# Kernel tuning notes

Hardware: AMD Instinct MI355X
Metric: run time of the kernel (lower is better)

Reference implementation:

```python
import jax, jax.numpy as jnp
import numpy as np

DETER, STOCH, ACT, HID, OBS = 1024, 32, 6, 1024, 1024
B, T = 256, 64

def _lin(x, w, b):
    return x @ w.T + b

def setup_inputs() -> dict:
    key = jax.random.key(0)
    ks = iter(jax.random.split(key, 40))
    def p(shape, scale=0.02):
        return (jax.random.normal(next(ks), shape, dtype=jnp.float32) * scale)
    inp = {
        "obs": jax.random.normal(next(ks), (B, T, OBS), dtype=jnp.float32),
        "actions": jax.random.normal(next(ks), (B, T, ACT), dtype=jnp.float32),
        "eps_prior": jax.random.normal(next(ks), (B, T, STOCH), dtype=jnp.float32),
        "eps_post": jax.random.normal(next(ks), (B, T, STOCH), dtype=jnp.float32),
        # input_mlp
        "in_w1": p((HID, STOCH + ACT)), "in_b1": p((HID,)),
        "in_w2": p((HID, HID)), "in_b2": p((HID,)),
        # GRUCell (torch layout: r,z,n chunks)
        "gru_wih": p((3 * DETER, HID)), "gru_whh": p((3 * DETER, DETER)),
        "gru_bih": p((3 * DETER,)), "gru_bhh": p((3 * DETER,)),
        # prior
        "pr_w1": p((HID, DETER)), "pr_b1": p((HID,)),
        "pr_w2": p((HID, HID)), "pr_b2": p((HID,)),
        "pr_mw": p((STOCH, HID)), "pr_mb": p((STOCH,)),
        "pr_sw": p((STOCH, HID)), "pr_sb": p((STOCH,)),
        # posterior
        "po_w1": p((HID, DETER + OBS)), "po_b1": p((HID,)),
        "po_w2": p((HID, HID)), "po_b2": p((HID,)),
        "po_mw": p((STOCH, HID)), "po_mb": p((STOCH,)),
        "po_sw": p((STOCH, HID)), "po_sb": p((STOCH,)),
    }
    return inp

def _rollout(obs, actions, eps_prior, eps_post,
             in_w1, in_b1, in_w2, in_b2,
             gru_wih, gru_whh, gru_bih, gru_bhh,
             pr_w1, pr_b1, pr_w2, pr_b2, pr_mw, pr_mb, pr_sw, pr_sb,
             po_w1, po_b1, po_w2, po_b2, po_mw, po_mb, po_sw, po_sb):
    Bn = obs.shape[0]
    h0 = jnp.zeros((Bn, DETER), obs.dtype)
    z0 = jnp.zeros((Bn, STOCH), obs.dtype)
    a0 = jnp.zeros((Bn, ACT), obs.dtype)

    def step(carry, xs):
        h, z, prev_a = carry
        obs_t, act_t, ep, eq = xs
        x = jnp.concatenate([z, prev_a], axis=-1)
        x = jax.nn.relu(_lin(x, in_w1, in_b1))
        x = jax.nn.relu(_lin(x, in_w2, in_b2))
        # GRUCell
        gi = _lin(x, gru_wih, gru_bih)
        gh = _lin(h, gru_whh, gru_bhh)
        ir, iz, inn = jnp.split(gi, 3, axis=-1)
        hr, hz, hn = jnp.split(gh, 3, axis=-1)
        r = jax.nn.sigmoid(ir + hr)
        u = jax.nn.sigmoid(iz + hz)
        n = jnp.tanh(inn + r * hn)
        h_new = (1.0 - u) * n + u * h
        # prior
        px = jax.nn.relu(_lin(h_new, pr_w1, pr_b1))
        px = jax.nn.relu(_lin(px, pr_w2, pr_b2))
        p_mean = _lin(px, pr_mw, pr_mb)
        p_std = jnp.exp(jnp.clip(_lin(px, pr_sw, pr_sb), -5.0, 2.0))
        # posterior
        qx = jnp.concatenate([h_new, obs_t], axis=-1)
        qx = jax.nn.relu(_lin(qx, po_w1, po_b1))
        qx = jax.nn.relu(_lin(qx, po_w2, po_b2))
        q_mean = _lin(qx, po_mw, po_mb)
        q_std = jnp.exp(jnp.clip(_lin(qx, po_sw, po_sb), -5.0, 2.0))
        z_new = q_mean + q_std * eq
        feat = jnp.concatenate([h_new, z_new], axis=-1)
        return (h_new, z_new, act_t), (feat, p_mean, p_std, q_mean, q_std)

    xs = (jnp.swapaxes(obs, 0, 1), jnp.swapaxes(actions, 0, 1),
          jnp.swapaxes(eps_prior, 0, 1), jnp.swapaxes(eps_post, 0, 1))
    _, (feat, pm, ps, qm, qs) = jax.lax.scan(step, (h0, z0, a0), xs)
    to_bt = lambda a: jnp.swapaxes(a, 0, 1)  # [T,B,...] -> [B,T,...]
    return to_bt(feat), to_bt(pm), to_bt(ps), to_bt(qm), to_bt(qs)

def reference(obs, actions, eps_prior, eps_post,
              in_w1, in_b1, in_w2, in_b2,
              gru_wih, gru_whh, gru_bih, gru_bhh,
              pr_w1, pr_b1, pr_w2, pr_b2, pr_mw, pr_mb, pr_sw, pr_sb,
              po_w1, po_b1, po_w2, po_b2, po_mw, po_mb, po_sw, po_sb):
    return _rollout(obs, actions, eps_prior, eps_post,
                    in_w1, in_b1, in_w2, in_b2,
                    gru_wih, gru_whh, gru_bih, gru_bhh,
                    pr_w1, pr_b1, pr_w2, pr_b2, pr_mw, pr_mb, pr_sw, pr_sb,
                    po_w1, po_b1, po_w2, po_b2, po_mw, po_mb, po_sw, po_sb)
```

## Files before the change

kernel.cpp:

```cpp
#include <hip/hip_runtime.h>
#include <hip/hip_bf16.h>

#define B_   256
#define T_   64
#define OBS_ 1024
#define ACT_ 6
#define STO_ 32
#define HID_ 1024
#define DET_ 1024

using bf16 = __bf16;
typedef __attribute__((ext_vector_type(8))) __bf16 bf16x8;
typedef __attribute__((ext_vector_type(4))) float f32x4;

__device__ __forceinline__ f32x4 MF(bf16x8 a, bf16x8 b, f32x4 c) {
  return __builtin_amdgcn_mfma_f32_16x16x32_bf16(a, b, c, 0, 0, 0);
}

struct CvtArgs {
  const float *in_w2, *gru_wih, *gru_whh, *pr_w1, *pr_w2, *po_w1, *po_w2;
  const float *pr_mw, *pr_sw, *po_mw, *po_sw;
  bf16 *w_in2b, *w_wihb, *w_whhb, *w_pr1b, *w_pr2b, *w_po1hb, *w_po1ob, *w_po2b, *w_headb;
};

__global__ void k_cvtall(CvtArgs a) {
  const int row = blockIdx.x;
  const float* src; bf16* dst; int srcld = 1024, off = 0;
  if      (row < 1024)  { src = a.in_w2   + (size_t)row * 1024;          dst = a.w_in2b  + (size_t)row * 1024; }
  else if (row < 4096)  { int r = row - 1024;  src = a.gru_wih + (size_t)r * 1024; dst = a.w_wihb + (size_t)r * 1024; }
  else if (row < 7168)  { int r = row - 4096;  src = a.gru_whh + (size_t)r * 1024; dst = a.w_whhb + (size_t)r * 1024; }
  else if (row < 8192)  { int r = row - 7168;  src = a.pr_w1   + (size_t)r * 1024; dst = a.w_pr1b + (size_t)r * 1024; }
  else if (row < 9216)  { int r = row - 8192;  src = a.pr_w2   + (size_t)r * 1024; dst = a.w_pr2b + (size_t)r * 1024; }
  else if (row < 10240) { int r = row - 9216;  src = a.po_w1   + (size_t)r * 2048; dst = a.w_po1hb + (size_t)r * 1024; }
  else if (row < 11264) { int r = row - 10240; src = a.po_w1   + (size_t)r * 2048 + 1024; dst = a.w_po1ob + (size_t)r * 1024; }
  else if (row < 12288) { int r = row - 11264; src = a.po_w2   + (size_t)r * 1024; dst = a.w_po2b + (size_t)r * 1024; }
  else {
    int r = row - 12288;
    const float* hs[4] = { a.pr_mw, a.pr_sw, a.po_mw, a.po_sw };
    src = hs[r >> 5] + (size_t)(r & 31) * 1024;
    dst = a.w_headb + (size_t)r * 1024;
  }
  const int c = threadIdx.x * 4;
  float4 f = *(const float4*)(src + c);
  dst[c] = (bf16)f.x; dst[c + 1] = (bf16)f.y; dst[c + 2] = (bf16)f.z; dst[c + 3] = (bf16)f.w;
}

__global__ void k_init(const float* __restrict__ in_b1, bf16* __restrict__ x1b,
                       bf16* __restrict__ hb, float* __restrict__ hf) {
  const int i = blockIdx.x * 256 + threadIdx.x;
  x1b[i] = (bf16)fmaxf(in_b1[i & 1023], 0.f);
  hb[i] = (bf16)0.f;
  hf[i] = 0.f;
}

__global__ __launch_bounds__(256) void k_qbatch(
    const float* __restrict__ obs, const bf16* __restrict__ w,
    const float* __restrict__ bias, float* __restrict__ out) {
  const int tid = threadIdx.x, lane = tid & 63, wv = tid >> 6;
  const int l15 = lane & 15, kg = lane >> 4, kq = kg * 8, rq = kg * 4;
  const int m0 = (blockIdx.x & 255) * 64 + wv * 16;
  const int n0 = (blockIdx.x >> 8) * 64;
  f32x4 c0{0.f,0.f,0.f,0.f}, c1 = c0, c2 = c0, c3 = c0;
  const float* __restrict__ ap = obs + (size_t)(m0 + l15) * 1024 + kq;
  const bf16* __restrict__ wp = w + (size_t)(n0 + l15) * 1024 + kq;
  #pragma unroll 2
  for (int k = 0; k < 1024; k += 32) {
    float4 f0 = *(const float4*)(ap + k);
    float4 f1 = *(const float4*)(ap + k + 4);
    bf16x8 af;
    af[0] = (bf16)f0.x; af[1] = (bf16)f0.y; af[2] = (bf16)f0.z; af[3] = (bf16)f0.w;
    af[4] = (bf16)f1.x; af[5] = (bf16)f1.y; af[6] = (bf16)f1.z; af[7] = (bf16)f1.w;
    c0 = MF(af, *(const bf16x8*)(wp + k            ), c0);
    c1 = MF(af, *(const bf16x8*)(wp + 16 * 1024 + k), c1);
    c2 = MF(af, *(const bf16x8*)(wp + 32 * 1024 + k), c2);
    c3 = MF(af, *(const bf16x8*)(wp + 48 * 1024 + k), c3);
  }
  f32x4 cc[4] = {c0, c1, c2, c3};
  #pragma unroll
  for (int t2 = 0; t2 < 4; ++t2) {
    const int n = n0 + t2 * 16 + l15;
    const float bv = bias[n];
    #pragma unroll
    for (int r = 0; r < 4; ++r)
      out[(size_t)(m0 + rq + r) * 1024 + n] = cc[t2][r] + bv;
  }
}

struct GB {
  const bf16* A;
  const bf16* W;
  const float* bias;
  const float* acc;
  bf16* outB;
  float* outF;
  int N, lda, relu, accStride;
};

__global__ __launch_bounds__(256, 4) void k_mgs(GB g0, GB g1, int s1) {
  GB g; int tile;
  if ((int)blockIdx.x < s1) { g = g0; tile = blockIdx.x; }
  else                      { g = g1; tile = blockIdx.x - s1; }
  __shared__ float sh[3 * 1056];
  const int tid = threadIdx.x, lane = tid & 63, kw = tid >> 6;
  const int l15 = lane & 15, kg = lane >> 4, kq = kg * 8, rq = kg * 4;
  const int m0 = (tile & 15) * 16;
  const int n0 = (tile >> 4) * 64;

  f32x4 c0{0.f,0.f,0.f,0.f}, c1 = c0, c2 = c0, c3 = c0;
  const bf16* __restrict__ ap = g.A + (size_t)(m0 + l15) * g.lda + kw * 256 + kq;
  const bf16* __restrict__ wp = g.W + (size_t)(n0 + l15) * 1024 + kw * 256 + kq;
  #pragma unroll
  for (int k = 0; k < 256; k += 32) {
    bf16x8 af = *(const bf16x8*)(ap + k);
    c0 = MF(af, *(const bf16x8*)(wp + k            ), c0);
    c1 = MF(af, *(const bf16x8*)(wp + 16 * 1024 + k), c1);
    c2 = MF(af, *(const bf16x8*)(wp + 32 * 1024 + k), c2);
    c3 = MF(af, *(const bf16x8*)(wp + 48 * 1024 + k), c3);
  }
  f32x4 cc[4] = {c0, c1, c2, c3};
  if (kw) {
    float* s = sh + (kw - 1) * 1056;
    #pragma unroll
    for (int t2 = 0; t2 < 4; ++t2)
      #pragma unroll
      for (int r = 0; r < 4; ++r)
        s[(rq + r) * 66 + t2 * 16 + l15] = cc[t2][r];
  }
  __syncthreads();
  if (kw == 0) {
    #pragma unroll
    for (int t2 = 0; t2 < 4; ++t2) {
      const int n = n0 + t2 * 16 + l15;
      const float bv = g.bias ? g.bias[n] : 0.f;
      #pragma unroll
      for (int r = 0; r < 4; ++r) {
        const int row = m0 + rq + r;
        float v = cc[t2][r] + bv;
        #pragma unroll
        for (int s = 0; s < 3; ++s)
          v += sh[s * 1056 + (rq + r) * 66 + t2 * 16 + l15];
        if (g.acc) v += g.acc[(size_t)row * g.accStride + n];
        if (g.relu) v = fmaxf(v, 0.f);
        if (g.outB) g.outB[(size_t)row * g.N + n] = (bf16)v;
        if (g.outF) g.outF[(size_t)row * g.N + n] = v;
      }
    }
  }
}

__global__ __launch_bounds__(256, 4) void k_gates2(
    const bf16* __restrict__ x2b, const bf16* __restrict__ wihb,
    const float* __restrict__ bih, const float* __restrict__ gh,
    float* __restrict__ hf, bf16* __restrict__ hb, float* __restrict__ feat, int t) {
  __shared__ float sh[3 * 816];
  const int mt = blockIdx.x & 15, cs = blockIdx.x >> 4;
  const int tid = threadIdx.x, lane = tid & 63, kw = tid >> 6;
  const int l15 = lane & 15, kg = lane >> 4, kq = kg * 8, rq = kg * 4;

  f32x4 ar{0.f,0.f,0.f,0.f}, az = ar, an = ar;
  const bf16* __restrict__ ap = x2b + (size_t)(mt * 16 + l15) * 1024 + kw * 256 + kq;
  const bf16* __restrict__ wr = wihb + (size_t)(cs * 16 + l15) * 1024 + kw * 256 + kq;
  const size_t GOFF = (size_t)1024 * 1024;
  #pragma unroll
  for (int k = 0; k < 256; k += 32) {
    bf16x8 af = *(const bf16x8*)(ap + k);
    ar = MF(af, *(const bf16x8*)(wr + k           ), ar);
    az = MF(af, *(const bf16x8*)(wr + GOFF + k    ), az);
    an = MF(af, *(const bf16x8*)(wr + 2 * GOFF + k), an);
  }
  if (kw) {
    float* s = sh + (kw - 1) * 816;
    #pragma unroll
    for (int r = 0; r < 4; ++r) {
      s[(rq + r) * 17 + l15]             = ar[r];
      s[272 + (rq + r) * 17 + l15]       = az[r];
      s[544 + (rq + r) * 17 + l15]       = an[r];
    }
  }
  __syncthreads();
  if (kw == 0) {
    const int c = cs * 16 + l15;
    const float bir = bih[c], biz = bih[1024 + c], bin_ = bih[2048 + c];
    #pragma unroll
    for (int r = 0; r < 4; ++r) {
      float vr = ar[r], vz = az[r], vn = an[r];
      #pragma unroll
      for (int s = 0; s < 3; ++s) {
        vr += sh[s * 816 + (rq + r) * 17 + l15];
        vz += sh[s * 816 + 272 + (rq + r) * 17 + l15];
        vn += sh[s * 816 + 544 + (rq + r) * 17 + l15];
      }
      const int m = mt * 16 + rq + r;
      const float* ghp = gh + (size_t)m * 3072 + c;
      float rr = vr + bir + ghp[0];
      float zz = vz + biz + ghp[1024];
      const float hn = ghp[2048];
      rr = 1.f / (1.f + __expf(-rr));
      zz = 1.f / (1.f + __expf(-zz));
      const float nn = tanhf(vn + bin_ + rr * hn);
      const float h2 = (1.f - zz) * nn + zz * hf[(size_t)m * 1024 + c];
      hf[(size_t)m * 1024 + c] = h2;
      hb[(size_t)m * 1024 + c] = (bf16)h2;
      feat[((size_t)m * T_ + t) * 1056 + c] = h2;
    }
  }
}

__global__ __launch_bounds__(1024, 1) void k_headfin2(
    const bf16* __restrict__ p2b, const bf16* __restrict__ q2b,
    const bf16* __restrict__ whead,
    const float* __restrict__ pr_mb, const float* __restrict__ pr_sb,
    const float* __restrict__ po_mb, const float* __restrict__ po_sb,
    const float* __restrict__ eps, const float* __restrict__ act,
    const float* __restrict__ in_w1, const float* __restrict__ in_b1,
    float* __restrict__ pm, float* __restrict__ ps,
    float* __restrict__ qm, float* __restrict__ qs,
    float* __restrict__ feat, bf16* __restrict__ x1b, int t) {
  __shared__ float sh[8 * 1056];
  __shared__ float zm[16][32], zs[16][32], zl[16][32], al[16][8];
  const int g = blockIdx.x, m0 = g * 16;
  const int tid = threadIdx.x, lane = tid & 63, w = tid >> 6;
  const int l15 = lane & 15, kg = lane >> 4, kq = kg * 8, rq = kg * 4;

  if (w < 8) {
    const int kw = w & 3, half = w >> 2;
    const bf16* __restrict__ A = half ? q2b : p2b;
    f32x4 c0{0.f,0.f,0.f,0.f}, c1 = c0, c2 = c0, c3 = c0;
    const bf16* __restrict__ ap = A + (size_t)(m0 + l15) * 1024 + kw * 256 + kq;
    const bf16* __restrict__ wp = whead + (size_t)(half * 64 + l15) * 1024 + kw * 256 + kq;
    #pragma unroll
    for (int k = 0; k < 256; k += 32) {
      bf16x8 af = *(const bf16x8*)(ap + k);
      c0 = MF(af, *(const bf16x8*)(wp + k            ), c0);
      c1 = MF(af, *(const bf16x8*)(wp + 16 * 1024 + k), c1);
      c2 = MF(af, *(const bf16x8*)(wp + 32 * 1024 + k), c2);
      c3 = MF(af, *(const bf16x8*)(wp + 48 * 1024 + k), c3);
    }
    f32x4 cc[4] = {c0, c1, c2, c3};
    float* s = sh + w * 1056;
    #pragma unroll
    for (int t2 = 0; t2 < 4; ++t2)
      #pragma unroll
      for (int r = 0; r < 4; ++r)
        s[(rq + r) * 66 + t2 * 16 + l15] = cc[t2][r];
  }
  if (tid >= 928 && tid < 1024) {
    const int idx = tid - 928, r = idx / ACT_, k = idx - r * ACT_;
    al[r][k] = act[((size_t)(m0 + r) * T_ + t) * ACT_ + k];
  }
  __syncthreads();

  #pragma unroll
  for (int rep = 0; rep < 2; ++rep) {
    const int idx = rep * 1024 + tid;
    const int r = idx >> 7, c = idx & 127;
    const int base = (c < 64) ? 0 : 4, cl = c & 63;
    float v = sh[base * 1056 + r * 66 + cl] + sh[(base + 1) * 1056 + r * 66 + cl]
            + sh[(base + 2) * 1056 + r * 66 + cl] + sh[(base + 3) * 1056 + r * 66 + cl];
    const size_t ob = ((size_t)(m0 + r) * T_ + t) * STO_ + (c & 31);
    const int sel = c >> 5;
    if (sel == 0) {
      pm[ob] = v + pr_mb[c];
    } else if (sel == 1) {
      ps[ob] = __expf(fminf(fmaxf(v + pr_sb[c - 32], -5.f), 2.f));
    } else if (sel == 2) {
      const float x = v + po_mb[c - 64];
      qm[ob] = x; zm[r][c - 64] = x;
    } else {
      const float x = __expf(fminf(fmaxf(v + po_sb[c - 96], -5.f), 2.f));
      qs[ob] = x; zs[r][c - 96] = x;
    }
  }
  __syncthreads();
  if (tid < 512) {
    const int r = tid >> 5, j = tid & 31;
    const float z = zm[r][j] + zs[r][j] * eps[((size_t)(m0 + r) * T_ + t) * STO_ + j];
    zl[r][j] = z;
    feat[((size_t)(m0 + r) * T_ + t) * 1056 + 1024 + j] = z;
  }
  __syncthreads();

  const int n = tid;
  float wv_[38];
  #pragma unroll
  for (int j = 0; j < 38; ++j) wv_[j] = in_w1[(size_t)n * 38 + j];
  const float bn = in_b1[n];
  #pragma unroll 2
  for (int r = 0; r < 16; ++r) {
    float a = bn;
    #pragma unroll
    for (int k = 0; k < STO_; ++k) a = fmaf(zl[r][k], wv_[k], a);
    #pragma unroll
    for (int k = 0; k < ACT_; ++k) a = fmaf(al[r][k], wv_[32 + k], a);
    x1b[(size_t)(m0 + r) * 1024 + n] = (bf16)fmaxf(a, 0.f);
  }
}

extern "C" void kernel_launch(void* const* d_in, const int* in_sizes, int n_in,
                              void* d_out, int out_size, void* d_ws, size_t ws_size,
                              hipStream_t stream) {
  (void)in_sizes; (void)n_in; (void)out_size; (void)ws_size;
  const float* obs      = (const float*)d_in[0];
  const float* actions  = (const float*)d_in[1];
  const float* eps_post = (const float*)d_in[3];
  const float* in_w1 = (const float*)d_in[4];
  const float* in_b1 = (const float*)d_in[5];
  const float* in_w2 = (const float*)d_in[6];
  const float* in_b2 = (const float*)d_in[7];
  const float* gru_wih = (const float*)d_in[8];
  const float* gru_whh = (const float*)d_in[9];
  const float* gru_bih = (const float*)d_in[10];
  const float* gru_bhh = (const float*)d_in[11];
  const float* pr_w1 = (const float*)d_in[12];
  const float* pr_b1 = (const float*)d_in[13];
  const float* pr_w2 = (const float*)d_in[14];
  const float* pr_b2 = (const float*)d_in[15];
  const float* pr_mw = (const float*)d_in[16];
  const float* pr_mb = (const float*)d_in[17];
  const float* pr_sw = (const float*)d_in[18];
  const float* pr_sb = (const float*)d_in[19];
  const float* po_w1 = (const float*)d_in[20];
  const float* po_b1 = (const float*)d_in[21];
  const float* po_w2 = (const float*)d_in[22];
  const float* po_b2 = (const float*)d_in[23];
  const float* po_mw = (const float*)d_in[24];
  const float* po_mb = (const float*)d_in[25];
  const float* po_sw = (const float*)d_in[26];
  const float* po_sb = (const float*)d_in[27];

  float* feat = (float*)d_out;
  float* pm = feat + (size_t)B_ * T_ * 1056;
  float* ps = pm + (size_t)B_ * T_ * STO_;
  float* qm = ps + (size_t)B_ * T_ * STO_;
  float* qs = qm + (size_t)B_ * T_ * STO_;

  char* wp_ = (char*)d_ws;
  auto carve = [&](size_t bytes) -> void* {
    void* r = (void*)wp_;
    wp_ += (bytes + 255) & ~(size_t)255;
    return r;
  };
  bf16* w_in2b  = (bf16*)carve((size_t)HID_ * HID_ * 2);
  bf16* w_wihb  = (bf16*)carve((size_t)3 * DET_ * HID_ * 2);
  bf16* w_whhb  = (bf16*)carve((size_t)3 * DET_ * DET_ * 2);
  bf16* w_pr1b  = (bf16*)carve((size_t)HID_ * DET_ * 2);
  bf16* w_pr2b  = (bf16*)carve((size_t)HID_ * HID_ * 2);
  bf16* w_po1hb = (bf16*)carve((size_t)HID_ * DET_ * 2);
  bf16* w_po1ob = (bf16*)carve((size_t)HID_ * OBS_ * 2);
  bf16* w_po2b  = (bf16*)carve((size_t)HID_ * HID_ * 2);
  bf16* w_headb = (bf16*)carve((size_t)128 * HID_ * 2);
  bf16* x1b  = (bf16*)carve((size_t)B_ * HID_ * 2);
  bf16* x2b  = (bf16*)carve((size_t)B_ * HID_ * 2);
  bf16* hb   = (bf16*)carve((size_t)B_ * DET_ * 2);
  bf16* p1b  = (bf16*)carve((size_t)B_ * HID_ * 2);
  bf16* q1b  = (bf16*)carve((size_t)B_ * HID_ * 2);
  bf16* p2b  = (bf16*)carve((size_t)B_ * HID_ * 2);
  bf16* q2b  = (bf16*)carve((size_t)B_ * HID_ * 2);
  float* hf       = (float*)carve((size_t)B_ * DET_ * 4);
  float* gh       = (float*)carve((size_t)B_ * 3 * DET_ * 4);
  float* q1acc    = (float*)carve((size_t)B_ * T_ * HID_ * 4);

  CvtArgs ca = { in_w2, gru_wih, gru_whh, pr_w1, pr_w2, po_w1, po_w2,
                 pr_mw, pr_sw, po_mw, po_sw,
                 w_in2b, w_wihb, w_whhb, w_pr1b, w_pr2b, w_po1hb, w_po1ob, w_po2b, w_headb };
  k_cvtall<<<dim3(12416), dim3(256), 0, stream>>>(ca);
  k_init<<<dim3(1024), dim3(256), 0, stream>>>(in_b1, x1b, hb, hf);
  k_qbatch<<<dim3(4096), dim3(256), 0, stream>>>(obs, w_po1ob, po_b1, q1acc);

  for (int t = 0; t < T_; ++t) {
    GB g_x2 = { x1b, w_in2b, in_b2,   nullptr, x2b, nullptr, 1024, 1024, 1, 0 };
    GB g_gh = { hb,  w_whhb, gru_bhh, nullptr, nullptr, gh, 3072, 1024, 0, 0 };
    k_mgs<<<dim3(1024), dim3(256), 0, stream>>>(g_x2, g_gh, 256);

    k_gates2<<<dim3(1024), dim3(256), 0, stream>>>(x2b, w_wihb, gru_bih, gh, hf, hb, feat, t);

    GB g_pr1 = { hb, w_pr1b,  pr_b1,   nullptr,           p1b, nullptr, 1024, 1024, 1, 0 };
    GB g_q1  = { hb, w_po1hb, nullptr, q1acc + t * 1024,  q1b, nullptr, 1024, 1024, 1, T_ * 1024 };
    k_mgs<<<dim3(512), dim3(256), 0, stream>>>(g_pr1, g_q1, 256);

    GB g_pr2 = { p1b, w_pr2b, pr_b2, nullptr, p2b, nullptr, 1024, 1024, 1, 0 };
    GB g_po2 = { q1b, w_po2b, po_b2, nullptr, q2b, nullptr, 1024, 1024, 1, 0 };
    k_mgs<<<dim3(512), dim3(256), 0, stream>>>(g_pr2, g_po2, 256);

    k_headfin2<<<dim3(16), dim3(1024), 0, stream>>>(
        p2b, q2b, w_headb, pr_mb, pr_sb, po_mb, po_sb,
        eps_post, actions, in_w1, in_b1, pm, ps, qm, qs, feat, x1b, t);
  }
}
```

Baseline: 6.055 ms.

## Fuse per-step kernels into one dataflow kernel with atomic counters

Replaces the four kernel launches per timestep with a single 240-block kernel. Block groups specialise by stage (input MLP, GRU, prior/posterior layers, heads) and hand off row tiles through global atomic counters instead of kernel boundaries. The GRU recurrent matmul runs before waiting on the input MLP, so the two overlap, and the h state is double-buffered so blocks can read the previous state while the new one is written. Correctness depends on all 240 blocks being co-resident, since waiting blocks spin, and each stage now runs on fewer, larger tiles with full-K loops and no split-K.

Result: slower. 15.04 ms (+148.3%).

```diff
diff --git a/kernel.cpp b/kernel.cpp
--- a/kernel.cpp
+++ b/kernel.cpp
@@ -7,7 +7,6 @@
 #define ACT_ 6
 #define STO_ 32
 #define HID_ 1024
-#define DET_ 1024
 
 using bf16 = __bf16;
 typedef __attribute__((ext_vector_type(8))) __bf16 bf16x8;
@@ -15,6 +14,272 @@
 
 __device__ __forceinline__ f32x4 MF(bf16x8 a, bf16x8 b, f32x4 c) {
   return __builtin_amdgcn_mfma_f32_16x16x32_bf16(a, b, c, 0, 0, 0);
+}
+
+__device__ __forceinline__ void waitctr(unsigned* c, unsigned tgt) {
+  if ((threadIdx.x & 63) == 0) {
+    while (__hip_atomic_load(c, __ATOMIC_RELAXED, __HIP_MEMORY_SCOPE_AGENT) < tgt)
+      __builtin_amdgcn_s_sleep(1);
+    __hip_atomic_load(c, __ATOMIC_ACQUIRE, __HIP_MEMORY_SCOPE_AGENT);
+  }
+  __builtin_amdgcn_wave_barrier();
+  asm volatile("" ::: "memory");
+}
+__device__ __forceinline__ void signalctr(unsigned* c) {
+  __syncthreads();
+  if (threadIdx.x == 0)
+    __hip_atomic_fetch_add(c, 1u, __ATOMIC_RELEASE, __HIP_MEMORY_SCOPE_AGENT);
+}
+
+__device__ __forceinline__ void gemm128(
+    const bf16* __restrict__ A, int m0,
+    const bf16* __restrict__ W,
+    const float* __restrict__ bias,
+    const float* __restrict__ accb, size_t accLd,
+    bf16* __restrict__ outb, int ldo) {
+  const int tid = threadIdx.x, lane = tid & 63, wv = tid >> 6;
+  const int l15 = lane & 15, kg = lane >> 4, kq = kg << 3, rq = kg << 2;
+  const int mrow = m0 + (wv & 3) * 16;
+  const int nb = (wv >> 2) * 64;
+  f32x4 a0{0.f,0.f,0.f,0.f}, a1 = a0, a2 = a0, a3 = a0;
+  const bf16* __restrict__ ap = A + (size_t)(mrow + l15) * 1024 + kq;
+  const bf16* __restrict__ wp = W + (size_t)(nb + l15) * 1024 + kq;
+  #pragma unroll 4
+  for (int k = 0; k < 1024; k += 32) {
+    bf16x8 af = *(const bf16x8*)(ap + k);
+    a0 = MF(af, *(const bf16x8*)(wp + k            ), a0);
+    a1 = MF(af, *(const bf16x8*)(wp + 16*1024 + k  ), a1);
+    a2 = MF(af, *(const bf16x8*)(wp + 32*1024 + k  ), a2);
+    a3 = MF(af, *(const bf16x8*)(wp + 48*1024 + k  ), a3);
+  }
+  f32x4 aa[4] = {a0, a1, a2, a3};
+  #pragma unroll
+  for (int nf = 0; nf < 4; ++nf) {
+    const int col = nb + nf * 16 + l15;
+    const float bv = bias ? bias[col] : 0.f;
+    #pragma unroll
+    for (int r = 0; r < 4; ++r) {
+      const int row = mrow + rq + r;
+      float v = aa[nf][r] + bv;
+      if (accb) v += accb[(size_t)row * accLd + col];
+      v = fmaxf(v, 0.f);
+      outb[(size_t)row * ldo + col] = (bf16)v;
+    }
+  }
+}
+
+struct SPar {
+  const bf16 *w_in2, *w_wih, *w_whh, *w_pr1, *w_po1h, *w_pr2, *w_po2, *w_head;
+  const float *b_in2, *b_ih, *b_hh, *b_pr1, *b_pr2, *b_po2;
+  const float *pr_mb, *pr_sb, *po_mb, *po_sb;
+  const float *eps, *act, *in_w1, *in_b1;
+  bf16 *x1b, *x2b, *p1b, *q1b, *p2b, *q2b, *hbA, *hbB;
+  float *hfA, *hfB;
+  const float *q1acc;
+  float *feat, *pm, *ps, *qm, *qs;
+  unsigned *ctr;
+};
+
+__global__ __launch_bounds__(512) void k_step(SPar P, int t) {
+  __shared__ float shmem[10048];
+  const int bid = blockIdx.x, tid = threadIdx.x;
+  const int lane = tid & 63, wv = tid >> 6;
+  const int l15 = lane & 15, kg = lane >> 4, kq = kg << 3, rq = kg << 2;
+  unsigned* cc = P.ctr + t * 32;
+  bf16* hbCur  = (t & 1) ? P.hbB : P.hbA;
+  const bf16* hbPrev = (t & 1) ? P.hbA : P.hbB;
+  float* hfCur = (t & 1) ? P.hfB : P.hfA;
+  const float* hfPrev = (t & 1) ? P.hfA : P.hfB;
+
+  if (bid < 32) {
+    const int mt = bid & 3, nt = bid >> 2;
+    gemm128(P.x1b, mt * 64, P.w_in2 + (size_t)nt * 128 * 1024,
+            P.b_in2 + nt * 128, nullptr, 0, P.x2b + nt * 128, 1024);
+    signalctr(&cc[0 * 4 + mt]);
+
+  } else if (bid < 96) {
+    const int idx = bid - 32, mt = idx & 3, cs = idx >> 2;
+    const int msub = wv & 3, nsh = wv >> 2;
+    const int mrow = mt * 64 + msub * 16;
+    const int cb = cs * 64 + nsh * 32;
+    f32x4 gh[3][2], gi[3][2];
+    #pragma unroll
+    for (int g = 0; g < 3; ++g)
+      #pragma unroll
+      for (int nf = 0; nf < 2; ++nf) { gh[g][nf] = f32x4{0.f,0.f,0.f,0.f}; gi[g][nf] = gh[g][nf]; }
+
+    {
+      const bf16* __restrict__ ap = hbPrev + (size_t)(mrow + l15) * 1024 + kq;
+      const bf16* wr[3][2];
+      #pragma unroll
+      for (int g = 0; g < 3; ++g)
+        #pragma unroll
+        for (int nf = 0; nf < 2; ++nf)
+          wr[g][nf] = P.w_whh + (size_t)(g * 1024 + cb + nf * 16 + l15) * 1024 + kq;
+      #pragma unroll 2
+      for (int k = 0; k < 1024; k += 32) {
+        bf16x8 af = *(const bf16x8*)(ap + k);
+        #pragma unroll
+        for (int g = 0; g < 3; ++g)
+          #pragma unroll
+          for (int nf = 0; nf < 2; ++nf)
+            gh[g][nf] = MF(af, *(const bf16x8*)(wr[g][nf] + k), gh[g][nf]);
+      }
+    }
+    waitctr(&cc[0 * 4 + mt], 8);
+    {
+      const bf16* __restrict__ ap = P.x2b + (size_t)(mrow + l15) * 1024 + kq;
+      const bf16* wr[3][2];
+      #pragma unroll
+      for (int g = 0; g < 3; ++g)
+        #pragma unroll
+        for (int nf = 0; nf < 2; ++nf)
+          wr[g][nf] = P.w_wih + (size_t)(g * 1024 + cb + nf * 16 + l15) * 1024 + kq;
+      #pragma unroll 2
+      for (int k = 0; k < 1024; k += 32) {
+        bf16x8 af = *(const bf16x8*)(ap + k);
+        #pragma unroll
+        for (int g = 0; g < 3; ++g)
+          #pragma unroll
+          for (int nf = 0; nf < 2; ++nf)
+            gi[g][nf] = MF(af, *(const bf16x8*)(wr[g][nf] + k), gi[g][nf]);
+      }
+    }
+    #pragma unroll
+    for (int nf = 0; nf < 2; ++nf) {
+      const int col = cb + nf * 16 + l15;
+      const float bir = P.b_ih[col], biz = P.b_ih[1024 + col], bin_ = P.b_ih[2048 + col];
+      const float bhr = P.b_hh[col], bhz = P.b_hh[1024 + col], bhn = P.b_hh[2048 + col];
+      #pragma unroll
+      for (int r = 0; r < 4; ++r) {
+        const int row = mrow + rq + r;
+        float rr = gi[0][nf][r] + bir + gh[0][nf][r] + bhr;
+        float zz = gi[1][nf][r] + biz + gh[1][nf][r] + bhz;
+        const float hn = gh[2][nf][r] + bhn;
+        rr = 1.f / (1.f + __expf(-rr));
+        zz = 1.f / (1.f + __expf(-zz));
+        const float nn = tanhf(gi[2][nf][r] + bin_ + rr * hn);
+        const float h2 = (1.f - zz) * nn + zz * hfPrev[(size_t)row * 1024 + col];
+        hbCur[(size_t)row * 1024 + col] = (bf16)h2;
+        hfCur[(size_t)row * 1024 + col] = h2;
+        P.feat[((size_t)row * T_ + t) * 1056 + col] = h2;
+      }
+    }
+    signalctr(&cc[1 * 4 + mt]);
+
+  } else if (bid < 128) {
+    const int idx = bid - 96, mt = idx & 3, nt = idx >> 2;
+    waitctr(&cc[1 * 4 + mt], 16);
+    gemm128(hbCur, mt * 64, P.w_po1h + (size_t)nt * 128 * 1024, nullptr,
+            P.q1acc + (size_t)t * 1024 + nt * 128, (size_t)T_ * 1024,
+            P.q1b + nt * 128, 1024);
+    signalctr(&cc[2 * 4 + mt]);
+
+  } else if (bid < 160) {
+    const int idx = bid - 128, mt = idx & 3, nt = idx >> 2;
+    waitctr(&cc[1 * 4 + mt], 16);
+    gemm128(hbCur, mt * 64, P.w_pr1 + (size_t)nt * 128 * 1024,
+            P.b_pr1 + nt * 128, nullptr, 0, P.p1b + nt * 128, 1024);
+    signalctr(&cc[3 * 4 + mt]);
+
+  } else if (bid < 192) {
+    const int idx = bid - 160, mt = idx & 3, nt = idx >> 2;
+    waitctr(&cc[2 * 4 + mt], 8);
+    gemm128(P.q1b, mt * 64, P.w_po2 + (size_t)nt * 128 * 1024,
+            P.b_po2 + nt * 128, nullptr, 0, P.q2b + nt * 128, 1024);
+    signalctr(&cc[4 * 4 + mt]);
+
+  } else if (bid < 224) {
+    const int idx = bid - 192, mt = idx & 3, nt = idx >> 2;
+    waitctr(&cc[3 * 4 + mt], 8);
+    gemm128(P.p1b, mt * 64, P.w_pr2 + (size_t)nt * 128 * 1024,
+            P.b_pr2 + nt * 128, nullptr, 0, P.p2b + nt * 128, 1024);
+    signalctr(&cc[5 * 4 + mt]);
+
+  } else {
+    const int g = bid - 224, m0 = g * 16, mt = g >> 2;
+    waitctr(&cc[4 * 4 + mt], 8);
+    waitctr(&cc[5 * 4 + mt], 8);
+    float* sh = shmem;
+    float* zm = shmem + 8448;
+    float* zs = zm + 512;
+    float* zl = zs + 512;
+    float* al = zl + 512;
+    {
+      const int kw = wv & 3, half = wv >> 2;
+      const bf16* __restrict__ A = half ? P.q2b : P.p2b;
+      f32x4 c0{0.f,0.f,0.f,0.f}, c1 = c0, c2 = c0, c3 = c0;
+      const bf16* __restrict__ ap = A + (size_t)(m0 + l15) * 1024 + kw * 256 + kq;
+      const bf16* __restrict__ wp = P.w_head + (size_t)(half * 64 + l15) * 1024 + kw * 256 + kq;
+      #pragma unroll
+      for (int k = 0; k < 256; k += 32) {
+        bf16x8 af = *(const bf16x8*)(ap + k);
+        c0 = MF(af, *(const bf16x8*)(wp + k            ), c0);
+        c1 = MF(af, *(const bf16x8*)(wp + 16*1024 + k  ), c1);
+        c2 = MF(af, *(const bf16x8*)(wp + 32*1024 + k  ), c2);
+        c3 = MF(af, *(const bf16x8*)(wp + 48*1024 + k  ), c3);
+      }
+      f32x4 ccx[4] = {c0, c1, c2, c3};
+      float* s = sh + wv * 1056;
+      #pragma unroll
+      for (int t2 = 0; t2 < 4; ++t2)
+        #pragma unroll
+        for (int r = 0; r < 4; ++r)
+          s[(rq + r) * 66 + t2 * 16 + l15] = ccx[t2][r];
+    }
+    if (tid < 96) {
+      const int r = tid / ACT_, k = tid - r * ACT_;
+      al[r * 8 + k] = P.act[((size_t)(m0 + r) * T_ + t) * ACT_ + k];
+    }
+    __syncthreads();
+    #pragma unroll
+    for (int rep = 0; rep < 4; ++rep) {
+      const int idx = rep * 512 + tid;
+      const int r = idx >> 7, c = idx & 127;
+      const int base = (c < 64) ? 0 : 4, cl = c & 63, j = c & 31;
+      float v = sh[base * 1056 + r * 66 + cl] + sh[(base + 1) * 1056 + r * 66 + cl]
+              + sh[(base + 2) * 1056 + r * 66 + cl] + sh[(base + 3) * 1056 + r * 66 + cl];
+      const size_t ob = ((size_t)(m0 + r) * T_ + t) * STO_ + j;
+      const int sel = c >> 5;
+      if (sel == 0) {
+        P.pm[ob] = v + P.pr_mb[j];
+      } else if (sel == 1) {
+        P.ps[ob] = __expf(fminf(fmaxf(v + P.pr_sb[j], -5.f), 2.f));
+      } else if (sel == 2) {
+        const float x = v + P.po_mb[j];
+        P.qm[ob] = x; zm[r * 32 + j] = x;
+      } else {
+        const float x = __expf(fminf(fmaxf(v + P.po_sb[j], -5.f), 2.f));
+        P.qs[ob] = x; zs[r * 32 + j] = x;
+      }
+    }
+    __syncthreads();
+    {
+      const int r = tid >> 5, j = tid & 31;
+      const float z = zm[r * 32 + j] + zs[r * 32 + j] * P.eps[((size_t)(m0 + r) * T_ + t) * STO_ + j];
+      zl[r * 32 + j] = z;
+      P.feat[((size_t)(m0 + r) * T_ + t) * 1056 + 1024 + j] = z;
+    }
+    __syncthreads();
+    #pragma unroll
+    for (int c2 = 0; c2 < 2; ++c2) {
+      const int n = c2 * 512 + tid;
+      const float* w = P.in_w1 + (size_t)n * 38;
+      float wreg[38];
+      #pragma unroll
+      for (int j = 0; j < 38; ++j) wreg[j] = w[j];
+      const float bn = P.in_b1[n];
+      #pragma unroll 2
+      for (int r = 0; r < 16; ++r) {
+        float a = bn;
+        #pragma unroll
+        for (int k = 0; k < STO_; ++k) a = fmaf(zl[r * 32 + k], wreg[k], a);
+        #pragma unroll
+        for (int k = 0; k < ACT_; ++k) a = fmaf(al[r * 8 + k], wreg[32 + k], a);
+        P.x1b[(size_t)(m0 + r) * 1024 + n] = (bf16)fmaxf(a, 0.f);
+      }
+    }
+  }
 }
 
 struct CvtArgs {
@@ -25,15 +290,15 @@
 
 __global__ void k_cvtall(CvtArgs a) {
   const int row = blockIdx.x;
-  const float* src; bf16* dst; int srcld = 1024, off = 0;
-  if      (row < 1024)  { src = a.in_w2   + (size_t)row * 1024;          dst = a.w_in2b  + (size_t)row * 1024; }
-  else if (row < 4096)  { int r = row - 1024;  src = a.gru_wih + (size_t)r * 1024; dst = a.w_wihb + (size_t)r * 1024; }
-  else if (row < 7168)  { int r = row - 4096;  src = a.gru_whh + (size_t)r * 1024; dst = a.w_whhb + (size_t)r * 1024; }
-  else if (row < 8192)  { int r = row - 7168;  src = a.pr_w1   + (size_t)r * 1024; dst = a.w_pr1b + (size_t)r * 1024; }
-  else if (row < 9216)  { int r = row - 8192;  src = a.pr_w2   + (size_t)r * 1024; dst = a.w_pr2b + (size_t)r * 1024; }
-  else if (row < 10240) { int r = row - 9216;  src = a.po_w1   + (size_t)r * 2048; dst = a.w_po1hb + (size_t)r * 1024; }
+  const float* src; bf16* dst;
+  if      (row < 1024)  { src = a.in_w2   + (size_t)row * 1024;               dst = a.w_in2b  + (size_t)row * 1024; }
+  else if (row < 4096)  { int r = row - 1024;  src = a.gru_wih + (size_t)r * 1024;        dst = a.w_wihb  + (size_t)r * 1024; }
+  else if (row < 7168)  { int r = row - 4096;  src = a.gru_whh + (size_t)r * 1024;        dst = a.w_whhb  + (size_t)r * 1024; }
+  else if (row < 8192)  { int r = row - 7168;  src = a.pr_w1   + (size_t)r * 1024;        dst = a.w_pr1b  + (size_t)r * 1024; }
+  else if (row < 9216)  { int r = row - 8192;  src = a.pr_w2   + (size_t)r * 1024;        dst = a.w_pr2b  + (size_t)r * 1024; }
+  else if (row < 10240) { int r = row - 9216;  src = a.po_w1   + (size_t)r * 2048;        dst = a.w_po1hb + (size_t)r * 1024; }
   else if (row < 11264) { int r = row - 10240; src = a.po_w1   + (size_t)r * 2048 + 1024; dst = a.w_po1ob + (size_t)r * 1024; }
-  else if (row < 12288) { int r = row - 11264; src = a.po_w2   + (size_t)r * 1024; dst = a.w_po2b + (size_t)r * 1024; }
+  else if (row < 12288) { int r = row - 11264; src = a.po_w2   + (size_t)r * 1024;        dst = a.w_po2b  + (size_t)r * 1024; }
   else {
     int r = row - 12288;
     const float* hs[4] = { a.pr_mw, a.pr_sw, a.po_mw, a.po_sw };
@@ -46,11 +311,12 @@
 }
 
 __global__ void k_init(const float* __restrict__ in_b1, bf16* __restrict__ x1b,
-                       bf16* __restrict__ hb, float* __restrict__ hf) {
+                       bf16* __restrict__ hbA, bf16* __restrict__ hbB,
+                       float* __restrict__ hfA, float* __restrict__ hfB) {
   const int i = blockIdx.x * 256 + threadIdx.x;
   x1b[i] = (bf16)fmaxf(in_b1[i & 1023], 0.f);
-  hb[i] = (bf16)0.f;
-  hf[i] = 0.f;
+  hbA[i] = (bf16)0.f; hbB[i] = (bf16)0.f;
+  hfA[i] = 0.f; hfB[i] = 0.f;
 }
 
 __global__ __launch_bounds__(256) void k_qbatch(
@@ -83,216 +349,6 @@
     #pragma unroll
     for (int r = 0; r < 4; ++r)
       out[(size_t)(m0 + rq + r) * 1024 + n] = cc[t2][r] + bv;
-  }
-}
-
-struct GB {
-  const bf16* A;
-  const bf16* W;
-  const float* bias;
-  const float* acc;
-  bf16* outB;
-  float* outF;
-  int N, lda, relu, accStride;
-};
-
-__global__ __launch_bounds__(256, 4) void k_mgs(GB g0, GB g1, int s1) {
-  GB g; int tile;
-  if ((int)blockIdx.x < s1) { g = g0; tile = blockIdx.x; }
-  else                      { g = g1; tile = blockIdx.x - s1; }
-  __shared__ float sh[3 * 1056];
-  const int tid = threadIdx.x, lane = tid & 63, kw = tid >> 6;
-  const int l15 = lane & 15, kg = lane >> 4, kq = kg * 8, rq = kg * 4;
-  const int m0 = (tile & 15) * 16;
-  const int n0 = (tile >> 4) * 64;
-
-  f32x4 c0{0.f,0.f,0.f,0.f}, c1 = c0, c2 = c0, c3 = c0;
-  const bf16* __restrict__ ap = g.A + (size_t)(m0 + l15) * g.lda + kw * 256 + kq;
-  const bf16* __restrict__ wp = g.W + (size_t)(n0 + l15) * 1024 + kw * 256 + kq;
-  #pragma unroll
-  for (int k = 0; k < 256; k += 32) {
-    bf16x8 af = *(const bf16x8*)(ap + k);
-    c0 = MF(af, *(const bf16x8*)(wp + k            ), c0);
-    c1 = MF(af, *(const bf16x8*)(wp + 16 * 1024 + k), c1);
-    c2 = MF(af, *(const bf16x8*)(wp + 32 * 1024 + k), c2);
-    c3 = MF(af, *(const bf16x8*)(wp + 48 * 1024 + k), c3);
-  }
-  f32x4 cc[4] = {c0, c1, c2, c3};
-  if (kw) {
-    float* s = sh + (kw - 1) * 1056;
-    #pragma unroll
-    for (int t2 = 0; t2 < 4; ++t2)
-      #pragma unroll
-      for (int r = 0; r < 4; ++r)
-        s[(rq + r) * 66 + t2 * 16 + l15] = cc[t2][r];
-  }
-  __syncthreads();
-  if (kw == 0) {
-    #pragma unroll
-    for (int t2 = 0; t2 < 4; ++t2) {
-      const int n = n0 + t2 * 16 + l15;
-      const float bv = g.bias ? g.bias[n] : 0.f;
-      #pragma unroll
-      for (int r = 0; r < 4; ++r) {
-        const int row = m0 + rq + r;
-        float v = cc[t2][r] + bv;
-        #pragma unroll
-        for (int s = 0; s < 3; ++s)
-          v += sh[s * 1056 + (rq + r) * 66 + t2 * 16 + l15];
-        if (g.acc) v += g.acc[(size_t)row * g.accStride + n];
-        if (g.relu) v = fmaxf(v, 0.f);
-        if (g.outB) g.outB[(size_t)row * g.N + n] = (bf16)v;
-        if (g.outF) g.outF[(size_t)row * g.N + n] = v;
-      }
-    }
-  }
-}
-
-__global__ __launch_bounds__(256, 4) void k_gates2(
-    const bf16* __restrict__ x2b, const bf16* __restrict__ wihb,
-    const float* __restrict__ bih, const float* __restrict__ gh,
-    float* __restrict__ hf, bf16* __restrict__ hb, float* __restrict__ feat, int t) {
-  __shared__ float sh[3 * 816];
-  const int mt = blockIdx.x & 15, cs = blockIdx.x >> 4;
-  const int tid = threadIdx.x, lane = tid & 63, kw = tid >> 6;
-  const int l15 = lane & 15, kg = lane >> 4, kq = kg * 8, rq = kg * 4;
-
-  f32x4 ar{0.f,0.f,0.f,0.f}, az = ar, an = ar;
-  const bf16* __restrict__ ap = x2b + (size_t)(mt * 16 + l15) * 1024 + kw * 256 + kq;
-  const bf16* __restrict__ wr = wihb + (size_t)(cs * 16 + l15) * 1024 + kw * 256 + kq;
-  const size_t GOFF = (size_t)1024 * 1024;
-  #pragma unroll
-  for (int k = 0; k < 256; k += 32) {
-    bf16x8 af = *(const bf16x8*)(ap + k);
-    ar = MF(af, *(const bf16x8*)(wr + k           ), ar);
-    az = MF(af, *(const bf16x8*)(wr + GOFF + k    ), az);
-    an = MF(af, *(const bf16x8*)(wr + 2 * GOFF + k), an);
-  }
-  if (kw) {
-    float* s = sh + (kw - 1) * 816;
-    #pragma unroll
-    for (int r = 0; r < 4; ++r) {
-      s[(rq + r) * 17 + l15]             = ar[r];
-      s[272 + (rq + r) * 17 + l15]       = az[r];
-      s[544 + (rq + r) * 17 + l15]       = an[r];
-    }
-  }
-  __syncthreads();
-  if (kw == 0) {
-    const int c = cs * 16 + l15;
-    const float bir = bih[c], biz = bih[1024 + c], bin_ = bih[2048 + c];
-    #pragma unroll
-    for (int r = 0; r < 4; ++r) {
-      float vr = ar[r], vz = az[r], vn = an[r];
-      #pragma unroll
-      for (int s = 0; s < 3; ++s) {
-        vr += sh[s * 816 + (rq + r) * 17 + l15];
-        vz += sh[s * 816 + 272 + (rq + r) * 17 + l15];
-        vn += sh[s * 816 + 544 + (rq + r) * 17 + l15];
-      }
-      const int m = mt * 16 + rq + r;
-      const float* ghp = gh + (size_t)m * 3072 + c;
-      float rr = vr + bir + ghp[0];
-      float zz = vz + biz + ghp[1024];
-      const float hn = ghp[2048];
-      rr = 1.f / (1.f + __expf(-rr));
-      zz = 1.f / (1.f + __expf(-zz));
-      const float nn = tanhf(vn + bin_ + rr * hn);
-      const float h2 = (1.f - zz) * nn + zz * hf[(size_t)m * 1024 + c];
-      hf[(size_t)m * 1024 + c] = h2;
-      hb[(size_t)m * 1024 + c] = (bf16)h2;
-      feat[((size_t)m * T_ + t) * 1056 + c] = h2;
-    }
-  }
-}
-
-__global__ __launch_bounds__(1024, 1) void k_headfin2(
-    const bf16* __restrict__ p2b, const bf16* __restrict__ q2b,
-    const bf16* __restrict__ whead,
-    const float* __restrict__ pr_mb, const float* __restrict__ pr_sb,
-    const float* __restrict__ po_mb, const float* __restrict__ po_sb,
-    const float* __restrict__ eps, const float* __restrict__ act,
-    const float* __restrict__ in_w1, const float* __restrict__ in_b1,
-    float* __restrict__ pm, float* __restrict__ ps,
-    float* __restrict__ qm, float* __restrict__ qs,
-    float* __restrict__ feat, bf16* __restrict__ x1b, int t) {
-  __shared__ float sh[8 * 1056];
-  __shared__ float zm[16][32], zs[16][32], zl[16][32], al[16][8];
-  const int g = blockIdx.x, m0 = g * 16;
-  const int tid = threadIdx.x, lane = tid & 63, w = tid >> 6;
-  const int l15 = lane & 15, kg = lane >> 4, kq = kg * 8, rq = kg * 4;
-
-  if (w < 8) {
-    const int kw = w & 3, half = w >> 2;
-    const bf16* __restrict__ A = half ? q2b : p2b;
-    f32x4 c0{0.f,0.f,0.f,0.f}, c1 = c0, c2 = c0, c3 = c0;
-    const bf16* __restrict__ ap = A + (size_t)(m0 + l15) * 1024 + kw * 256 + kq;
-    const bf16* __restrict__ wp = whead + (size_t)(half * 64 + l15) * 1024 + kw * 256 + kq;
-    #pragma unroll
-    for (int k = 0; k < 256; k += 32) {
-      bf16x8 af = *(const bf16x8*)(ap + k);
-      c0 = MF(af, *(const bf16x8*)(wp + k            ), c0);
-      c1 = MF(af, *(const bf16x8*)(wp + 16 * 1024 + k), c1);
-      c2 = MF(af, *(const bf16x8*)(wp + 32 * 1024 + k), c2);
-      c3 = MF(af, *(const bf16x8*)(wp + 48 * 1024 + k), c3);
-    }
-    f32x4 cc[4] = {c0, c1, c2, c3};
-    float* s = sh + w * 1056;
-    #pragma unroll
-    for (int t2 = 0; t2 < 4; ++t2)
-      #pragma unroll
-      for (int r = 0; r < 4; ++r)
-        s[(rq + r) * 66 + t2 * 16 + l15] = cc[t2][r];
-  }
-  if (tid >= 928 && tid < 1024) {
-    const int idx = tid - 928, r = idx / ACT_, k = idx - r * ACT_;
-    al[r][k] = act[((size_t)(m0 + r) * T_ + t) * ACT_ + k];
-  }
-  __syncthreads();
-
-  #pragma unroll
-  for (int rep = 0; rep < 2; ++rep) {
-    const int idx = rep * 1024 + tid;
-    const int r = idx >> 7, c = idx & 127;
-    const int base = (c < 64) ? 0 : 4, cl = c & 63;
-    float v = sh[base * 1056 + r * 66 + cl] + sh[(base + 1) * 1056 + r * 66 + cl]
-            + sh[(base + 2) * 1056 + r * 66 + cl] + sh[(base + 3) * 1056 + r * 66 + cl];
-    const size_t ob = ((size_t)(m0 + r) * T_ + t) * STO_ + (c & 31);
-    const int sel = c >> 5;
-    if (sel == 0) {
-      pm[ob] = v + pr_mb[c];
-    } else if (sel == 1) {
-      ps[ob] = __expf(fminf(fmaxf(v + pr_sb[c - 32], -5.f), 2.f));
-    } else if (sel == 2) {
-      const float x = v + po_mb[c - 64];
-      qm[ob] = x; zm[r][c - 64] = x;
-    } else {
-      const float x = __expf(fminf(fmaxf(v + po_sb[c - 96], -5.f), 2.f));
-      qs[ob] = x; zs[r][c - 96] = x;
-    }
-  }
-  __syncthreads();
-  if (tid < 512) {
-    const int r = tid >> 5, j = tid & 31;
-    const float z = zm[r][j] + zs[r][j] * eps[((size_t)(m0 + r) * T_ + t) * STO_ + j];
-    zl[r][j] = z;
-    feat[((size_t)(m0 + r) * T_ + t) * 1056 + 1024 + j] = z;
-  }
-  __syncthreads();
-
-  const int n = tid;
-  float wv_[38];
-  #pragma unroll
-  for (int j = 0; j < 38; ++j) wv_[j] = in_w1[(size_t)n * 38 + j];
-  const float bn = in_b1[n];
-  #pragma unroll 2
-  for (int r = 0; r < 16; ++r) {
-    float a = bn;
-    #pragma unroll
-    for (int k = 0; k < STO_; ++k) a = fmaf(zl[r][k], wv_[k], a);
-    #pragma unroll
-    for (int k = 0; k < ACT_; ++k) a = fmaf(al[r][k], wv_[32 + k], a);
-    x1b[(size_t)(m0 + r) * 1024 + n] = (bf16)fmaxf(a, 0.f);
   }
 }
 
@@ -341,49 +397,49 @@
     return r;
   };
   bf16* w_in2b  = (bf16*)carve((size_t)HID_ * HID_ * 2);
-  bf16* w_wihb  = (bf16*)carve((size_t)3 * DET_ * HID_ * 2);
-  bf16* w_whhb  = (bf16*)carve((size_t)3 * DET_ * DET_ * 2);
-  bf16* w_pr1b  = (bf16*)carve((size_t)HID_ * DET_ * 2);
+  bf16* w_wihb  = (bf16*)carve((size_t)3 * HID_ * HID_ * 2);
+  bf16* w_whhb  = (bf16*)carve((size_t)3 * HID_ * HID_ * 2);
+  bf16* w_pr1b  = (bf16*)carve((size_t)HID_ * HID_ * 2);
   bf16* w_pr2b  = (bf16*)carve((size_t)HID_ * HID_ * 2);
-  bf16* w_po1hb = (bf16*)carve((size_t)HID_ * DET_ * 2);
+  bf16* w_po1hb = (bf16*)carve((size_t)HID_ * HID_ * 2);
   bf16* w_po1ob = (bf16*)carve((size_t)HID_ * OBS_ * 2);
   bf16* w_po2b  = (bf16*)carve((size_t)HID_ * HID_ * 2);
   bf16* w_headb = (bf16*)carve((size_t)128 * HID_ * 2);
-  bf16* x1b  = (bf16*)carve((size_t)B_ * HID_ * 2);
-  bf16* x2b  = (bf16*)carve((size_t)B_ * HID_ * 2);
-  bf16* hb   = (bf16*)carve((size_t)B_ * DET_ * 2);
-  bf16* p1b  = (bf16*)carve((size_t)B_ * HID_ * 2);
-  bf16* q1b  = (bf16*)carve((size_t)B_ * HID_ * 2);
-  bf16* p2b  = (bf16*)carve((size_t)B_ * HID_ * 2);
-  bf16* q2b  = (bf16*)carve((size_t)B_ * HID_ * 2);
-  float* hf       = (float*)carve((size_t)B_ * DET_ * 4);
-  float* gh       = (float*)carve((size_t)B_ * 3 * DET_ * 4);
-  float* q1acc    = (float*)carve((size_t)B_ * T_ * HID_ * 4);
+  bf16* x1b = (bf16*)carve((size_t)B_ * HID_ * 2);
+  bf16* x2b = (bf16*)carve((size_t)B_ * HID_ * 2);
+  bf16* hbA = (bf16*)carve((size_t)B_ * HID_ * 2);
+  bf16* hbB = (bf16*)carve((size_t)B_ * HID_ * 2);
+  bf16* p1b = (bf16*)carve((size_t)B_ * HID_ * 2);
+  bf16* q1b = (bf16*)carve((size_t)B_ * HID_ * 2);
+  bf16* p2b = (bf16*)carve((size_t)B_ * HID_ * 2);
+  bf16* q2b = (bf16*)carve((size_t)B_ * HID_ * 2);
+  float* hfA = (float*)carve((size_t)B_ * HID_ * 4);
+  float* hfB = (float*)carve((size_t)B_ * HID_ * 4);
+  float* q1acc = (float*)carve((size_t)B_ * T_ * HID_ * 4);
+  unsigned* ctr = (unsigned*)carve((size_t)T_ * 32 * 4);
+
+  hipMemsetAsync(ctr, 0, (size_t)T_ * 32 * 4, stream);
 
   CvtArgs ca = { in_w2, gru_wih, gru_whh, pr_w1, pr_w2, po_w1, po_w2,
                  pr_mw, pr_sw, po_mw, po_sw,
                  w_in2b, w_wihb, w_whhb, w_pr1b, w_pr2b, w_po1hb, w_po1ob, w_po2b, w_headb };
   k_cvtall<<<dim3(12416), dim3(256), 0, stream>>>(ca);
-  k_init<<<dim3(1024), dim3(256), 0, stream>>>(in_b1, x1b, hb, hf);
+  k_init<<<dim3(1024), dim3(256), 0, stream>>>(in_b1, x1b, hbA, hbB, hfA, hfB);
   k_qbatch<<<dim3(4096), dim3(256), 0, stream>>>(obs, w_po1ob, po_b1, q1acc);
 
-  for (int t = 0; t < T_; ++t) {
-    GB g_x2 = { x1b, w_in2b, in_b2,   nullptr, x2b, nullptr, 1024, 1024, 1, 0 };
-    GB g_gh = { hb,  w_whhb, gru_bhh, nullptr, nullptr, gh, 3072, 1024, 0, 0 };
-    k_mgs<<<dim3(1024), dim3(256), 0, stream>>>(g_x2, g_gh, 256);
-
-    k_gates2<<<dim3(1024), dim3(256), 0, stream>>>(x2b, w_wihb, gru_bih, gh, hf, hb, feat, t);
-
-    GB g_pr1 = { hb, w_pr1b,  pr_b1,   nullptr,           p1b, nullptr, 1024, 1024, 1, 0 };
-    GB g_q1  = { hb, w_po1hb, nullptr, q1acc + t * 1024,  q1b, nullptr, 1024, 1024, 1, T_ * 1024 };
-    k_mgs<<<dim3(512), dim3(256), 0, stream>>>(g_pr1, g_q1, 256);
-
-    GB g_pr2 = { p1b, w_pr2b, pr_b2, nullptr, p2b, nullptr, 1024, 1024, 1, 0 };
-    GB g_po2 = { q1b, w_po2b, po_b2, nullptr, q2b, nullptr, 1024, 1024, 1, 0 };
-    k_mgs<<<dim3(512), dim3(256), 0, stream>>>(g_pr2, g_po2, 256);
-
-    k_headfin2<<<dim3(16), dim3(1024), 0, stream>>>(
-        p2b, q2b, w_headb, pr_mb, pr_sb, po_mb, po_sb,
-        eps_post, actions, in_w1, in_b1, pm, ps, qm, qs, feat, x1b, t);
-  }
-}
+  SPar P;
+  P.w_in2 = w_in2b; P.w_wih = w_wihb; P.w_whh = w_whhb; P.w_pr1 = w_pr1b;
+  P.w_po1h = w_po1hb; P.w_pr2 = w_pr2b; P.w_po2 = w_po2b; P.w_head = w_headb;
+  P.b_in2 = in_b2; P.b_ih = gru_bih; P.b_hh = gru_bhh;
+  P.b_pr1 = pr_b1; P.b_pr2 = pr_b2; P.b_po2 = po_b2;
+  P.pr_mb = pr_mb; P.pr_sb = pr_sb; P.po_mb = po_mb; P.po_sb = po_sb;
+  P.eps = eps_post; P.act = actions; P.in_w1 = in_w1; P.in_b1 = in_b1;
+  P.x1b = x1b; P.x2b = x2b; P.p1b = p1b; P.q1b = q1b; P.p2b = p2b; P.q2b = q2b;
+  P.hbA = hbA; P.hbB = hbB; P.hfA = hfA; P.hfB = hfB;
+  P.q1acc = q1acc;
+  P.feat = feat; P.pm = pm; P.ps = ps; P.qm = qm; P.qs = qs;
+  P.ctr = ctr;
+
+  for (int t = 0; t < T_; ++t)
+    k_step<<<dim3(240), dim3(512), 0, stream>>>(P, t);
+}
```
